# Kernel optimization log

Hardware: AMD Instinct MI355X
Metric: run time of the kernel (lower is better)

The kernel has to match this reference:

```python
import jax, jax.numpy as jnp
import numpy as np

NB_LABELS = 64
BOS = 61
EOS = 62
PAD = 63


def setup_inputs() -> dict:
    key = jax.random.key(0)
    k1, k2, k3 = jax.random.split(key, 3)
    B, S, L = 512, 1024, NB_LABELS
    emissions = jax.random.normal(k1, (B, S, L), dtype=jnp.float32)
    tags = jax.random.randint(k2, (B, S), 0, 61)  # avoid BOS/EOS/PAD ids
    mask = jnp.ones((B, S), dtype=jnp.float32)
    # transitions initialized as in CRF.init_weights()
    trans = jax.random.uniform(k3, (L, L), jnp.float32, -0.1, 0.1)
    trans = trans.at[:, BOS].set(-10000.0)
    trans = trans.at[EOS, :].set(-10000.0)
    trans = trans.at[PAD, :].set(-10000.0)
    trans = trans.at[:, PAD].set(-10000.0)
    trans = trans.at[PAD, EOS].set(0.0)
    trans = trans.at[PAD, PAD].set(0.0)
    return {"emissions": emissions, "transitions": trans, "tags": tags, "mask": mask}


def _gold_scores(emissions, transitions, tags, mask):
    # fully vectorized version of _compute_scores (no time loop needed)
    first_tags = tags[:, 0]
    last_idx = mask.astype(jnp.int32).sum(1) - 1  # (B,)
    last_tags = jnp.take_along_axis(tags, last_idx[:, None], axis=1)[:, 0]
    scores = transitions[BOS, first_tags]
    scores = scores + jnp.take_along_axis(emissions[:, 0], first_tags[:, None], axis=1)[:, 0]
    e = jnp.take_along_axis(emissions[:, 1:], tags[:, 1:, None], axis=2)[:, :, 0]  # (B,S-1)
    t = transitions[tags[:, :-1], tags[:, 1:]]  # (B,S-1)
    scores = scores + ((e + t) * mask[:, 1:]).sum(axis=1)
    scores = scores + transitions[last_tags, EOS]
    return scores


def _log_partition(emissions, transitions, mask):
    # forward algorithm via lax.scan; state alphas: (B, L)
    alpha0 = transitions[BOS][None, :] + emissions[:, 0]

    def step(alphas, xs):
        em_t, m_t = xs  # (B, L), (B,)
        # scores[b, prev, cur] = alphas[b, prev] + transitions[prev, cur] + em_t[b, cur]
        new = jax.nn.logsumexp(alphas[:, :, None] + transitions[None, :, :] + em_t[:, None, :], axis=1)
        alphas = m_t[:, None] * new + (1.0 - m_t[:, None]) * alphas
        return alphas, None

    xs = (jnp.swapaxes(emissions[:, 1:], 0, 1), jnp.swapaxes(mask[:, 1:], 0, 1))
    alphas, _ = jax.lax.scan(step, alpha0, xs)
    return jax.nn.logsumexp(alphas + transitions[:, EOS][None, :], axis=1)


def reference(emissions, transitions, tags, mask):
    scores = _gold_scores(emissions, transitions, tags, mask)
    partition = _log_partition(emissions, transitions, mask)
    # forward() returns the negative log-likelihood per batch element
    return partition - scores
```

## Files before the change

### kernel.cpp

```cpp
#include <hip/hip_runtime.h>
#include <hip/hip_bf16.h>

#define CRF_B 512
#define CRF_S 1024
#define CRF_L 64
#define CRF_BOS 61
#define CRF_EOS 62
#define CRF_NC 64
#define CRF_CK (CRF_S / CRF_NC)
#define CRF_W 4
#define GRP 16
#define PART_BLOCKS ((CRF_B / GRP) * CRF_NC)

typedef __attribute__((ext_vector_type(8))) short short8;
typedef __attribute__((ext_vector_type(4))) float f32x4;
#define UNR _Pragma("unroll")

__device__ __forceinline__ unsigned short f2bf(float x) {
    union { __hip_bfloat16 h; unsigned short u; } cv;
    cv.h = __float2bfloat16(x);
    return cv.u;
}

__device__ __forceinline__ void gold_body(
    int b, int l,
    const float* __restrict__ em, const float* __restrict__ trans,
    const int* __restrict__ tags, const float* __restrict__ mask,
    float* __restrict__ out)
{
    const float* emb = em + (size_t)b * CRF_S * CRF_L;
    const int*   tg  = tags + (size_t)b * CRF_S;
    const float* mk  = mask + (size_t)b * CRF_S;

    float acc = 0.f, msum = 0.f;
    for (int t = l; t < CRF_S; t += 64) {
        float m = mk[t];
        msum += m;
        if (t >= 1) {
            int ct = tg[t];
            int pt = tg[t - 1];
            acc += (emb[(size_t)t * CRF_L + ct] + trans[pt * CRF_L + ct]) * m;
        }
    }
    UNR
    for (int off = 32; off; off >>= 1) {
        acc  += __shfl_xor(acc, off);
        msum += __shfl_xor(msum, off);
    }
    if (l == 0) {
        int t0 = tg[0];
        acc += trans[CRF_BOS * CRF_L + t0] + emb[t0];
        int last = (int)(msum + 0.5f) - 1;
        int lt = tg[last];
        acc += trans[lt * CRF_L + CRF_EOS];
        atomicAdd(&out[b], -acc);
    }
}


#define STEP(T, eeU, eeV, rawU, mU)                                             \
  {                                                                             \
    short8 Bf0, Bf1;                                                            \
    UNR for (int e = 0; e < 8; ++e) {                                           \
        Bf0[e] = (short)f2bf(val[e >> 2][e & 3]);                               \
        Bf1[e] = (short)f2bf(val[2 + (e >> 2)][e & 3]);                         \
    }                                                                           \
    UNR for (int mt = 0; mt < 4; ++mt) {                                        \
        f32x4 acc = {0.f, 0.f, 0.f, 0.f};                                       \
        acc = __builtin_amdgcn_mfma_f32_16x16x32_bf16(Af[mt][0], Bf0, acc, 0, 0, 0); \
        acc = __builtin_amdgcn_mfma_f32_16x16x32_bf16(Af[mt][1], Bf1, acc, 0, 0, 0); \
        UNR for (int r = 0; r < 4; ++r) {                                       \
            float nv = acc[r] * eeU[mt * 4 + r];                                \
            val[mt][r] = (mU > 0.5f) ? nv : val[mt][r];                         \
        }                                                                       \
    }                                                                           \
                          \
    UNR for (int i = 0; i < 16; ++i) eeV[i] = __expf(rawU[i]);                  \
                       \
    { int tl = (T) + 3; if (tl > CRF_S - 1) tl = CRF_S - 1;                     \
      int tm = (T) + 2; if (tm > te) tm = te;                                   \
      mU = mrow[tm];                                                            \
      UNR for (int mt = 0; mt < 4; ++mt) {                                      \
          f32x4 rv = *(const f32x4*)(erow + (size_t)tl * CRF_L + mt * 16);      \
          UNR for (int r = 0; r < 4; ++r) rawU[mt * 4 + r] = rv[r];             \
      } }                                                                       \
    if (((T) & 7) == 0) {                                                       \
        float rsc = __shfl(val[0][0], l & 15);                                  \
        Clog += __logf(rsc);                                                    \
        float inv = 1.0f / rsc;                                                 \
        UNR for (int mt = 0; mt < 4; ++mt)                                      \
            UNR for (int r = 0; r < 4; ++r) val[mt][r] *= inv;                  \
    }                                                                           \
    if ((T) == t_mid) a0 = Clog + __logf(__shfl(val[0][0], l & 15));            \
  }

__device__ __forceinline__ void part_body(
    int pb, int l,
    const float* __restrict__ em, const float* __restrict__ trans,
    const float* __restrict__ mask, float* __restrict__ out)
{
    const int c   = pb & (CRF_NC - 1);
    const int grp = pb / CRF_NC;
    const int lj  = l & 15;
    const int g   = l >> 4;

    short8 Af[4][2];
    UNR for (int mt = 0; mt < 4; ++mt)
      UNR for (int kc = 0; kc < 2; ++kc) {
        short8 f;
        UNR for (int e = 0; e < 8; ++e) {
            int L = kc * 32 + (e >> 2) * 16 + g * 4 + (e & 3);
            f[e] = (short)f2bf(__expf(trans[L * CRF_L + mt * 16 + lj]));
        }
        Af[mt][kc] = f;
      }

    const int b = grp * GRP + lj;
    const float* erow = em + (size_t)b * (CRF_S * CRF_L) + g * 4;
    const float* mrow = mask + (size_t)b * CRF_S;

    const int t_mid = CRF_CK * c;
    int t1, te;
    float val[4][4];
    if (c == 0) {
        t1 = 1; te = CRF_CK;
        UNR for (int mt = 0; mt < 4; ++mt)
          UNR for (int r = 0; r < 4; ++r) {
            int n = mt * 16 + g * 4 + r;
            val[mt][r] = __expf(trans[CRF_BOS * CRF_L + n] + erow[mt * 16 + r]);
          }
    } else {
        t1 = t_mid - CRF_W + 1;
        te = (c == CRF_NC - 1) ? (CRF_S - 1) : (t_mid + CRF_CK);
        UNR for (int mt = 0; mt < 4; ++mt)
          UNR for (int r = 0; r < 4; ++r) val[mt][r] = 1.0f;
    }

    float Clog = 0.f, a0 = 0.f;

    float eeX[16], eeY[16], rawX[16], rawY[16], mX, mY;
    mX = mrow[t1];
    { int tn = t1 + 1; if (tn > te) tn = te; mY = mrow[tn]; }
    UNR for (int mt = 0; mt < 4; ++mt) {
        f32x4 r0 = *(const f32x4*)(erow + (size_t)t1 * CRF_L + mt * 16);
        int ta = t1 + 1; if (ta > CRF_S - 1) ta = CRF_S - 1;
        int tb = t1 + 2; if (tb > CRF_S - 1) tb = CRF_S - 1;
        f32x4 r1 = *(const f32x4*)(erow + (size_t)ta * CRF_L + mt * 16);
        f32x4 r2 = *(const f32x4*)(erow + (size_t)tb * CRF_L + mt * 16);
        UNR for (int r = 0; r < 4; ++r) {
            eeX[mt * 4 + r]  = __expf(r0[r]);
            rawX[mt * 4 + r] = r1[r];
            rawY[mt * 4 + r] = r2[r];
        }
    }

    int t = t1;
    for (; t + 1 <= te; t += 2) {
        STEP(t,     eeX, eeY, rawX, mX);
        STEP(t + 1, eeY, eeX, rawY, mY);
    }
    if (t <= te) STEP(t, eeX, eeY, rawX, mX);

    float a1;
    if (c == CRF_NC - 1) {
        float s = 0.f;
        UNR for (int mt = 0; mt < 4; ++mt)
          UNR for (int r = 0; r < 4; ++r)
            s += val[mt][r] * __expf(trans[(mt * 16 + g * 4 + r) * CRF_L + CRF_EOS]);
        s += __shfl_xor(s, 16);
        s += __shfl_xor(s, 32);
        a1 = Clog + __logf(s);
    } else {
        a1 = Clog + __logf(__shfl(val[0][0], l & 15));
    }
    if (l < 16) atomicAdd(&out[b], a1 - a0);
}

__global__ __launch_bounds__(64) void crf_fused(
    const float* __restrict__ em, const float* __restrict__ trans,
    const int* __restrict__ tags, const float* __restrict__ mask,
    float* __restrict__ out)
{
    const int bid = blockIdx.x;
    const int l   = threadIdx.x;
    if (bid < PART_BLOCKS) {
        part_body(bid, l, em, trans, mask, out);
    } else {
        gold_body(bid - PART_BLOCKS, l, em, trans, tags, mask, out);
    }
}

extern "C" void kernel_launch(void* const* d_in, const int* in_sizes, int n_in,
                              void* d_out, int out_size, void* d_ws, size_t ws_size,
                              hipStream_t stream) {
    const float* em    = (const float*)d_in[0];
    const float* trans = (const float*)d_in[1];
    const int*   tags  = (const int*)d_in[2];
    const float* mask  = (const float*)d_in[3];
    float* out  = (float*)d_out;

    hipMemsetAsync(out, 0, CRF_B * sizeof(float), stream);
    crf_fused<<<PART_BLOCKS + CRF_B, 64, 0, stream>>>(em, trans, tags, mask, out);
}
```

Baseline: 50.62 us.

## Stage emissions through LDS with async global_load_lds double buffering

The forward-algorithm chunks now load emission and mask tiles of four timesteps into shared memory with direct global-to-LDS loads, double buffered and using an XOR swizzle. This replaces the per-lane register prefetch of strided rows. It also halves the chunk count to 32 and widens the warm-up window to 8 steps. The intent is coalesced, latency-hidden loads. In exchange each block handles more sequential steps, there are fewer blocks, and waits rely on a hand-coded vmcnt, which is fragile.

```diff
diff --git a/kernel.cpp b/kernel.cpp
--- a/kernel.cpp
+++ b/kernel.cpp
@@ -6,11 +6,12 @@
 #define CRF_L 64
 #define CRF_BOS 61
 #define CRF_EOS 62
-#define CRF_NC 64
+#define CRF_NC 32
 #define CRF_CK (CRF_S / CRF_NC)
-#define CRF_W 4
+#define CRF_W 8
 #define GRP 16
 #define PART_BLOCKS ((CRF_B / GRP) * CRF_NC)
+#define TS 4
 
 typedef __attribute__((ext_vector_type(8))) short short8;
 typedef __attribute__((ext_vector_type(4))) float f32x4;
@@ -20,6 +21,17 @@
     union { __hip_bfloat16 h; unsigned short u; } cv;
     cv.h = __float2bfloat16(x);
     return cv.u;
+}
+
+__device__ __forceinline__ void gload_lds16(const float* g, float* l) {
+    __builtin_amdgcn_global_load_lds(
+        (const __attribute__((address_space(1))) unsigned int*)(const void*)g,
+        (__attribute__((address_space(3))) unsigned int*)(void*)l, 16, 0, 0);
+}
+__device__ __forceinline__ void gload_lds4(const float* g, float* l) {
+    __builtin_amdgcn_global_load_lds(
+        (const __attribute__((address_space(1))) unsigned int*)(const void*)g,
+        (__attribute__((address_space(3))) unsigned int*)(void*)l, 4, 0, 0);
 }
 
 __device__ __forceinline__ void gold_body(
@@ -57,47 +69,12 @@
     }
 }
 
-
-#define STEP(T, eeU, eeV, rawU, mU)                                             \
-  {                                                                             \
-    short8 Bf0, Bf1;                                                            \
-    UNR for (int e = 0; e < 8; ++e) {                                           \
-        Bf0[e] = (short)f2bf(val[e >> 2][e & 3]);                               \
-        Bf1[e] = (short)f2bf(val[2 + (e >> 2)][e & 3]);                         \
-    }                                                                           \
-    UNR for (int mt = 0; mt < 4; ++mt) {                                        \
-        f32x4 acc = {0.f, 0.f, 0.f, 0.f};                                       \
-        acc = __builtin_amdgcn_mfma_f32_16x16x32_bf16(Af[mt][0], Bf0, acc, 0, 0, 0); \
-        acc = __builtin_amdgcn_mfma_f32_16x16x32_bf16(Af[mt][1], Bf1, acc, 0, 0, 0); \
-        UNR for (int r = 0; r < 4; ++r) {                                       \
-            float nv = acc[r] * eeU[mt * 4 + r];                                \
-            val[mt][r] = (mU > 0.5f) ? nv : val[mt][r];                         \
-        }                                                                       \
-    }                                                                           \
-                          \
-    UNR for (int i = 0; i < 16; ++i) eeV[i] = __expf(rawU[i]);                  \
-                       \
-    { int tl = (T) + 3; if (tl > CRF_S - 1) tl = CRF_S - 1;                     \
-      int tm = (T) + 2; if (tm > te) tm = te;                                   \
-      mU = mrow[tm];                                                            \
-      UNR for (int mt = 0; mt < 4; ++mt) {                                      \
-          f32x4 rv = *(const f32x4*)(erow + (size_t)tl * CRF_L + mt * 16);      \
-          UNR for (int r = 0; r < 4; ++r) rawU[mt * 4 + r] = rv[r];             \
-      } }                                                                       \
-    if (((T) & 7) == 0) {                                                       \
-        float rsc = __shfl(val[0][0], l & 15);                                  \
-        Clog += __logf(rsc);                                                    \
-        float inv = 1.0f / rsc;                                                 \
-        UNR for (int mt = 0; mt < 4; ++mt)                                      \
-            UNR for (int r = 0; r < 4; ++r) val[mt][r] *= inv;                  \
-    }                                                                           \
-    if ((T) == t_mid) a0 = Clog + __logf(__shfl(val[0][0], l & 15));            \
-  }
-
 __device__ __forceinline__ void part_body(
     int pb, int l,
     const float* __restrict__ em, const float* __restrict__ trans,
-    const float* __restrict__ mask, float* __restrict__ out)
+    const float* __restrict__ mask, float* __restrict__ out,
+    float (* __restrict__ em_s)[GRP][TS][CRF_L],
+    float (* __restrict__ mk_s)[TS][GRP])
 {
     const int c   = pb & (CRF_NC - 1);
     const int grp = pb / CRF_NC;
@@ -115,19 +92,19 @@
         Af[mt][kc] = f;
       }
 
-    const int b = grp * GRP + lj;
-    const float* erow = em + (size_t)b * (CRF_S * CRF_L) + g * 4;
-    const float* mrow = mask + (size_t)b * CRF_S;
+    const int b0 = grp * GRP;
+    const int b  = b0 + lj;
 
     const int t_mid = CRF_CK * c;
     int t1, te;
     float val[4][4];
     if (c == 0) {
         t1 = 1; te = CRF_CK;
+        const float* erow0 = em + (size_t)b * (CRF_S * CRF_L);
         UNR for (int mt = 0; mt < 4; ++mt)
           UNR for (int r = 0; r < 4; ++r) {
             int n = mt * 16 + g * 4 + r;
-            val[mt][r] = __expf(trans[CRF_BOS * CRF_L + n] + erow[mt * 16 + r]);
+            val[mt][r] = __expf(trans[CRF_BOS * CRF_L + n] + erow0[n]);
           }
     } else {
         t1 = t_mid - CRF_W + 1;
@@ -135,31 +112,87 @@
         UNR for (int mt = 0; mt < 4; ++mt)
           UNR for (int r = 0; r < 4; ++r) val[mt][r] = 1.0f;
     }
+    const int NT = (te - t1 + TS) / TS;
+
+    auto issue_tile = [&](int k) {
+        const int tt0 = t1 + k * TS;
+        const int buf = k & 1;
+        int ttl = tt0 + (l >> 4); if (ttl > CRF_S - 1) ttl = CRF_S - 1;
+        UNR for (int bb = 0; bb < GRP; ++bb) {
+            const float* src = em + ((size_t)(b0 + bb) * CRF_S + ttl) * CRF_L
+                             + 4 * ((l & 15) ^ bb);
+            gload_lds16(src, &em_s[buf][bb][0][0]);
+        }
+        const float* msrc = mask + (size_t)(b0 + (l & 15)) * CRF_S + ttl;
+        gload_lds4(msrc, &mk_s[buf][0][0]);
+    };
 
     float Clog = 0.f, a0 = 0.f;
 
-    float eeX[16], eeY[16], rawX[16], rawY[16], mX, mY;
-    mX = mrow[t1];
-    { int tn = t1 + 1; if (tn > te) tn = te; mY = mrow[tn]; }
-    UNR for (int mt = 0; mt < 4; ++mt) {
-        f32x4 r0 = *(const f32x4*)(erow + (size_t)t1 * CRF_L + mt * 16);
-        int ta = t1 + 1; if (ta > CRF_S - 1) ta = CRF_S - 1;
-        int tb = t1 + 2; if (tb > CRF_S - 1) tb = CRF_S - 1;
-        f32x4 r1 = *(const f32x4*)(erow + (size_t)ta * CRF_L + mt * 16);
-        f32x4 r2 = *(const f32x4*)(erow + (size_t)tb * CRF_L + mt * 16);
-        UNR for (int r = 0; r < 4; ++r) {
-            eeX[mt * 4 + r]  = __expf(r0[r]);
-            rawX[mt * 4 + r] = r1[r];
-            rawY[mt * 4 + r] = r2[r];
-        }
-    }
-
-    int t = t1;
-    for (; t + 1 <= te; t += 2) {
-        STEP(t,     eeX, eeY, rawX, mX);
-        STEP(t + 1, eeY, eeX, rawY, mY);
-    }
-    if (t <= te) STEP(t, eeX, eeY, rawX, mX);
+    issue_tile(0);
+    if (NT > 1) issue_tile(1);
+
+    for (int k = 0; k < NT; ++k) {
+        const int buf = k & 1;
+        const int tt0 = t1 + k * TS;
+
+        if (k + 2 <= NT) {
+            asm volatile("s_waitcnt vmcnt(17)" ::: "memory");
+        } else {
+            asm volatile("s_waitcnt vmcnt(0)" ::: "memory");
+        }
+        __builtin_amdgcn_sched_barrier(0);
+
+        f32x4 rc[4]; float mc;
+        UNR for (int mt = 0; mt < 4; ++mt)
+            rc[mt] = *(const f32x4*)((const char*)&em_s[buf][lj][0][0]
+                                     + (((mt * 4 + g) ^ lj) << 4));
+        mc = mk_s[buf][0][lj];
+
+        UNR for (int dt = 0; dt < TS; ++dt) {
+            const int t = tt0 + dt;
+            if (t > te) break;
+            f32x4 rn[4]; float mn;
+            if (dt + 1 < TS) {
+                UNR for (int mt = 0; mt < 4; ++mt)
+                    rn[mt] = *(const f32x4*)((const char*)&em_s[buf][lj][dt + 1][0]
+                                             + (((mt * 4 + g) ^ lj) << 4));
+                mn = mk_s[buf][dt + 1][lj];
+            }
+            float ee[16];
+            UNR for (int mt = 0; mt < 4; ++mt)
+                UNR for (int r = 0; r < 4; ++r)
+                    ee[mt * 4 + r] = __expf(rc[mt][r]);
+
+            short8 Bf0, Bf1;
+            UNR for (int e = 0; e < 8; ++e) {
+                Bf0[e] = (short)f2bf(val[e >> 2][e & 3]);
+                Bf1[e] = (short)f2bf(val[2 + (e >> 2)][e & 3]);
+            }
+            UNR for (int mt = 0; mt < 4; ++mt) {
+                f32x4 acc = {0.f, 0.f, 0.f, 0.f};
+                acc = __builtin_amdgcn_mfma_f32_16x16x32_bf16(Af[mt][0], Bf0, acc, 0, 0, 0);
+                acc = __builtin_amdgcn_mfma_f32_16x16x32_bf16(Af[mt][1], Bf1, acc, 0, 0, 0);
+                UNR for (int r = 0; r < 4; ++r) {
+                    float nv = acc[r] * ee[mt * 4 + r];
+                    val[mt][r] = (mc > 0.5f) ? nv : val[mt][r];
+                }
+            }
+            if ((t & 7) == 0) {
+                float rsc = __shfl(val[0][0], l & 15);
+                Clog += __logf(rsc);
+                float inv = 1.0f / rsc;
+                UNR for (int mt = 0; mt < 4; ++mt)
+                    UNR for (int r = 0; r < 4; ++r) val[mt][r] *= inv;
+            }
+            if (t == t_mid) a0 = Clog + __logf(__shfl(val[0][0], l & 15));
+            if (dt + 1 < TS) {
+                UNR for (int mt = 0; mt < 4; ++mt) rc[mt] = rn[mt];
+                mc = mn;
+            }
+        }
+        if (k + 2 < NT) issue_tile(k + 2);
+    }
 
     float a1;
     if (c == CRF_NC - 1) {
@@ -181,10 +214,12 @@
     const int* __restrict__ tags, const float* __restrict__ mask,
     float* __restrict__ out)
 {
+    __shared__ float em_s[2][GRP][TS][CRF_L];
+    __shared__ float mk_s[2][TS][GRP];
     const int bid = blockIdx.x;
     const int l   = threadIdx.x;
     if (bid < PART_BLOCKS) {
-        part_body(bid, l, em, trans, mask, out);
+        part_body(bid, l, em, trans, mask, out, em_s, mk_s);
     } else {
         gold_body(bid - PART_BLOCKS, l, em, trans, tags, mask, out);
     }
```

Result: no change. 51.21 us (+1.2%).
